# Kernel tuning notes

Measured on AMD Instinct MI355X. Metric: run time of the kernel, lower is better.

## Reference

```python
import jax, jax.numpy as jnp
import numpy as np

DIM = 1024
NUM_HEADS = 16
HEAD_DIM = DIM // NUM_HEADS


def setup_inputs() -> dict:
    key = jax.random.key(0)
    k1, k2, k3, k4, k5 = jax.random.split(key, 5)
    B, N, C = 8, 1024, DIM
    x = jax.random.normal(k1, (B, N, C), dtype=jnp.float32)
    s_in = 1.0 / np.sqrt(C)
    w_qkv = jax.random.normal(k2, (C, 3 * C), dtype=jnp.float32) * s_in
    b_qkv = jnp.zeros((3 * C,), dtype=jnp.float32)
    w_proj = jax.random.normal(k3, (C, C), dtype=jnp.float32) * s_in
    b_proj = jnp.zeros((C,), dtype=jnp.float32)
    return {"x": x, "w_qkv": w_qkv, "b_qkv": b_qkv, "w_proj": w_proj, "b_proj": b_proj}


def reference(x, w_qkv, b_qkv, w_proj, b_proj):
    B, N, C = x.shape
    H, D = NUM_HEADS, C // NUM_HEADS
    scale = jnp.float32(1.0) / jnp.sqrt(jnp.float32(D))
    qkv = x @ w_qkv + b_qkv                      # [B, N, 3C]
    qkv = qkv.reshape(B, N, 3, H, D)
    qkv = jnp.transpose(qkv, (2, 0, 3, 1, 4))     # [3, B, H, N, D]
    q, k, v = qkv[0], qkv[1], qkv[2]
    attn = jnp.einsum('bhnd,bhmd->bhnm', q, k) * scale  # [B, H, N, N]
    attn = jax.nn.softmax(attn, axis=-1)
    out = jnp.einsum('bhnm,bhmd->bhnd', attn, v)  # [B, H, N, D]
    out = jnp.transpose(out, (0, 2, 1, 3)).reshape(B, N, C)
    return out @ w_proj + b_proj
```

## Files before the change

### kernel.cpp

```cpp
#include <hip/hip_runtime.h>
#include <stdint.h>
#include <stddef.h>


#define DEVI __device__ __forceinline__

typedef float f32x4 __attribute__((ext_vector_type(4)));
typedef float f32x16 __attribute__((ext_vector_type(16)));
typedef __bf16 bf16x8 __attribute__((ext_vector_type(8)));
typedef unsigned short u16x8 __attribute__((ext_vector_type(8)));
typedef unsigned short u16x4 __attribute__((ext_vector_type(4)));
typedef unsigned int u32;
typedef unsigned int u32x4 __attribute__((ext_vector_type(4)));

static constexpr int M1 = 8192;

DEVI unsigned short f2bf(float f) {
  uint32_t u = __builtin_bit_cast(uint32_t, f);
  u += 0x7FFFu + ((u >> 16) & 1u);
  return (unsigned short)(u >> 16);
}

DEVI float fexp2(float x) {
  float r;
  asm("v_exp_f32 %0, %1" : "=v"(r) : "v"(x));
  return r;
}

DEVI u32 cvtpk(float lo, float hi) {
  u32 r;
  asm("v_cvt_pk_bf16_f32 %0, %1, %2" : "=v"(r) : "v"(lo), "v"(hi));
  return r;
}

DEVI void plswap(u32& a, u32& b) {
  asm("v_permlane32_swap_b32 %0, %1" : "+v"(a), "+v"(b));
}

DEVI void gll16(const unsigned short* g, unsigned short* lds) {
  __builtin_amdgcn_global_load_lds(
      (const __attribute__((address_space(1))) void*)g,
      (__attribute__((address_space(3))) void*)lds, 16, 0, 0);
}

DEVI bf16x8 lds_frag(const unsigned short* p) {
  return __builtin_bit_cast(bf16x8, *(const u16x8*)p);
}

__global__ void k_cvt(const float* __restrict__ in, unsigned short* __restrict__ out, int n4) {
  int i = blockIdx.x * blockDim.x + threadIdx.x;
  if (i < n4) {
    float4 v = reinterpret_cast<const float4*>(in)[i];
    u16x4 o = { f2bf(v.x), f2bf(v.y), f2bf(v.z), f2bf(v.w) };
    reinterpret_cast<u16x4*>(out)[i] = o;
  }
}

__global__ void k_tr_cvt(const float* __restrict__ in, unsigned short* __restrict__ out,
                         int R, int Cc) {
  __shared__ float tile[32][33];
  int c0 = blockIdx.x * 32, r0 = blockIdx.y * 32;
  int tx = threadIdx.x, ty = threadIdx.y;
#pragma unroll
  for (int j = 0; j < 32; j += 8)
    tile[ty + j][tx] = in[(size_t)(r0 + ty + j) * Cc + c0 + tx];
  __syncthreads();
#pragma unroll
  for (int j = 0; j < 32; j += 8)
    out[(size_t)(c0 + ty + j) * R + r0 + tx] = f2bf(tile[tx][ty + j]);
}

template <int EPI, int NCOLS>
__global__ __launch_bounds__(256, 2)
void k_gemm(const unsigned short* __restrict__ A,
            const unsigned short* __restrict__ Bt,
            const float* __restrict__ bias,
            unsigned short* __restrict__ Qp,
            unsigned short* __restrict__ Kp,
            unsigned short* __restrict__ Vtp,
            float* __restrict__ Out) {
  constexpr int K = 1024, NK = K / 32;
  __shared__ unsigned short As[2][128 * 32];
  __shared__ unsigned short Bs[2][128 * 32];

  const int tid = threadIdx.x;
  const int w = tid >> 6, l = tid & 63;
  const int ln = l & 15, kg = l >> 4;
  const int wr = w >> 1, wc = w & 1;

  const int rt = blockIdx.x % (M1 / 128);
  const int ct = blockIdx.x / (M1 / 128);
  const int row0 = rt * 128, col0 = ct * 128;

  f32x4 acc[4][4] = {};

  const unsigned short* Ag = A + (size_t)row0 * K;
  const unsigned short* Bg = Bt + (size_t)col0 * K;

  auto stage = [&](int buf, int kt) {
    const unsigned short* ga = Ag + kt * 32;
    const unsigned short* gb = Bg + kt * 32;
#pragma unroll
    for (int j = 0; j < 2; j++) {
      int c = j * 256 + w * 64 + l;
      int r = c >> 2, s = c & 3;
      int ss = s ^ ((r >> 1) & 3);
      gll16(ga + (size_t)r * K + ss * 8, &As[buf][(j * 256 + w * 64) * 8]);
      gll16(gb + (size_t)r * K + ss * 8, &Bs[buf][(j * 256 + w * 64) * 8]);
    }
  };

  stage(0, 0);
  __syncthreads();

  int buf = 0;
  for (int kt = 0; kt < NK; kt++) {
    if (kt + 1 < NK) stage(buf ^ 1, kt + 1);

    bf16x8 af[4], bfr[4];
#pragma unroll
    for (int m = 0; m < 4; m++) {
      int r = wr * 64 + m * 16 + ln;
      int sl = kg ^ ((r >> 1) & 3);
      af[m] = lds_frag(&As[buf][r * 32 + sl * 8]);
    }
#pragma unroll
    for (int n = 0; n < 4; n++) {
      int r = wc * 64 + n * 16 + ln;
      int sl = kg ^ ((r >> 1) & 3);
      bfr[n] = lds_frag(&Bs[buf][r * 32 + sl * 8]);
    }
    __builtin_amdgcn_s_setprio(1);
#pragma unroll
    for (int m = 0; m < 4; m++)
#pragma unroll
      for (int n = 0; n < 4; n++)
        acc[m][n] = __builtin_amdgcn_mfma_f32_16x16x32_bf16(af[m], bfr[n], acc[m][n], 0, 0, 0);
    __builtin_amdgcn_s_setprio(0);

    __syncthreads();
    buf ^= 1;
  }

  constexpr float QS = 0.18033688011112042f;
  float bv[4];
#pragma unroll
  for (int n = 0; n < 4; n++) bv[n] = bias[col0 + wc * 64 + n * 16 + ln];

  if constexpr (EPI == 1) {
    const int three = col0 >> 10;
    const int h = ((col0 & 1023) >> 6) + wc;
    if (three < 2) {
      unsigned short* tgt = (three == 0) ? Qp : Kp;
      const float sc = (three == 0) ? QS : 1.f;
#pragma unroll
      for (int m = 0; m < 4; m++)
#pragma unroll
        for (int r = 0; r < 4; r++) {
          int row = row0 + wr * 64 + m * 16 + kg * 4 + r;
          int bb = row >> 10, nn = row & 1023;
          size_t base = ((size_t)(bb * 16 + h) * 1024 + nn) * 64;
#pragma unroll
          for (int n = 0; n < 4; n++)
            tgt[base + n * 16 + ln] = f2bf((acc[m][n][r] + bv[n]) * sc);
        }
    } else {
#pragma unroll
      for (int m = 0; m < 4; m++)
#pragma unroll
        for (int r = 0; r < 4; r++) {
          int row = row0 + wr * 64 + m * 16 + kg * 4 + r;
          int bb = row >> 10, nn = row & 1023;
          size_t dbase = (size_t)(bb * 16 + h) * 64;
#pragma unroll
          for (int n = 0; n < 4; n++)
            Vtp[(dbase + n * 16 + ln) * 1024 + nn] = f2bf(acc[m][n][r] + bv[n]);
        }
    }
  } else {
#pragma unroll
    for (int m = 0; m < 4; m++)
#pragma unroll
      for (int r = 0; r < 4; r++) {
        int row = row0 + wr * 64 + m * 16 + kg * 4 + r;
#pragma unroll
        for (int n = 0; n < 4; n++)
          Out[(size_t)row * 1024 + col0 + wc * 64 + n * 16 + ln] = acc[m][n][r] + bv[n];
      }
  }
}

__global__ __launch_bounds__(256, 4)
void k_attn(const unsigned short* __restrict__ Qg, const unsigned short* __restrict__ Kg,
            const unsigned short* __restrict__ Vtg, unsigned short* __restrict__ AO) {
  __shared__ unsigned short Ks[2][64 * 64];
  __shared__ unsigned short Vs[2][64 * 64];

  const int tid = threadIdx.x;
  const int w = tid >> 6, l = tid & 63;
  const int lq = l & 31, b = l >> 5;

  const int bh = blockIdx.x;
  const int qt = blockIdx.y;
  const int qbase = qt * 128 + w * 32;

  bf16x8 qf[4];
#pragma unroll
  for (int kk = 0; kk < 4; kk++) {
    size_t off = ((size_t)bh * 1024 + qbase + lq) * 64 + kk * 16 + b * 8;
    qf[kk] = __builtin_bit_cast(bf16x8, *(const u16x8*)(Qg + off));
  }

  f32x16 acc[2] = {};
  float mrun = -1e30f, lrun = 0.f;

  const unsigned short* Kbh = Kg + (size_t)bh * 1024 * 64;
  const unsigned short* Vbh = Vtg + (size_t)bh * 64 * 1024;

  auto stage = [&](int buf, int t) {
#pragma unroll
    for (int j = 0; j < 2; j++) {
      int c = j * 256 + w * 64 + l;
      int r = c >> 3, s = c & 7;
      int ss = s ^ (r & 7);
      gll16(Kbh + (size_t)(t * 64 + r) * 64 + ss * 8, &Ks[buf][(j * 256 + w * 64) * 8]);
      gll16(Vbh + (size_t)r * 1024 + t * 64 + ss * 8, &Vs[buf][(j * 256 + w * 64) * 8]);
    }
  };

  stage(0, 0);
  __syncthreads();

  int buf = 0;
  for (int t = 0; t < 16; t++) {
    if (t + 1 < 16) stage(buf ^ 1, t + 1);

    f32x16 s[2];
    __builtin_amdgcn_s_setprio(1);
#pragma unroll
    for (int kb = 0; kb < 2; kb++) {
      f32x16 z = {};
#pragma unroll
      for (int kk = 0; kk < 4; kk++) {
        int row = kb * 32 + lq;
        int ss = (kk * 2 + b) ^ (row & 7);
        bf16x8 kf = lds_frag(&Ks[buf][row * 64 + ss * 8]);
        z = __builtin_amdgcn_mfma_f32_32x32x16_bf16(kf, qf[kk], z, 0, 0, 0);
      }
      s[kb] = z;
    }
    __builtin_amdgcn_s_setprio(0);

    float tm = s[0][0];
#pragma unroll
    for (int kb = 0; kb < 2; kb++)
#pragma unroll
      for (int r = 0; r < 16; r++) tm = fmaxf(tm, s[kb][r]);
    tm = fmaxf(tm, __shfl_xor(tm, 32));

    if (!__all(tm <= mrun + 8.f)) {
      float mnew = fmaxf(mrun, tm);
      float al = fexp2(mrun - mnew);
      mrun = mnew;
      lrun *= al;
#pragma unroll
      for (int r = 0; r < 16; r++) {
        float aq = __shfl(al, (r & 3) + 8 * (r >> 2) + 4 * b);
        acc[0][r] *= aq;
        acc[1][r] *= aq;
      }
    }

    float rs = 0.f;
#pragma unroll
    for (int kb = 0; kb < 2; kb++)
#pragma unroll
      for (int r = 0; r < 16; r++) {
        float pv = fexp2(s[kb][r] - mrun);
        s[kb][r] = pv;
        rs += pv;
      }
    rs += __shfl_xor(rs, 32);
    lrun += rs;

    bf16x8 pa[4];
#pragma unroll
    for (int kb = 0; kb < 2; kb++) {
      u32 pk[4][2];
#pragma unroll
      for (int t4 = 0; t4 < 4; t4++) {
        pk[t4][0] = cvtpk(s[kb][t4 * 4 + 0], s[kb][t4 * 4 + 1]);
        pk[t4][1] = cvtpk(s[kb][t4 * 4 + 2], s[kb][t4 * 4 + 3]);
      }
#pragma unroll
      for (int sh = 0; sh < 2; sh++) {
        u32 a0 = pk[2 * sh][0], b0 = pk[2 * sh + 1][0];
        plswap(a0, b0);
        u32 a1 = pk[2 * sh][1], b1 = pk[2 * sh + 1][1];
        plswap(a1, b1);
        u32x4 fr = { a0, a1, b0, b1 };
        pa[kb * 2 + sh] = __builtin_bit_cast(bf16x8, fr);
      }
    }

    __builtin_amdgcn_s_setprio(1);
#pragma unroll
    for (int n = 0; n < 2; n++) {
#pragma unroll
      for (int st = 0; st < 4; st++) {
        int row = n * 32 + lq;
        int ss = (st * 2 + b) ^ (row & 7);
        bf16x8 vb = lds_frag(&Vs[buf][row * 64 + ss * 8]);
        acc[n] = __builtin_amdgcn_mfma_f32_32x32x16_bf16(pa[st], vb, acc[n], 0, 0, 0);
      }
    }
    __builtin_amdgcn_s_setprio(0);

    __syncthreads();
    buf ^= 1;
  }

  const int bb = bh >> 4, h = bh & 15;
  float linv = 1.f / lrun;
#pragma unroll
  for (int r = 0; r < 16; r++) {
    float lq_r = __shfl(linv, (r & 3) + 8 * (r >> 2) + 4 * b);
    int row = qbase + (r & 3) + 8 * (r >> 2) + 4 * b;
    size_t base = ((size_t)(bb * 1024 + row)) * 1024 + h * 64;
#pragma unroll
    for (int n = 0; n < 2; n++)
      AO[base + n * 32 + lq] = f2bf(acc[n][r] * lq_r);
  }
}

extern "C" void kernel_launch(void* const* d_in, const int* in_sizes, int n_in,
                              void* d_out, int out_size, void* d_ws, size_t ws_size,
                              hipStream_t stream) {
  const float* x      = (const float*)d_in[0];
  const float* w_qkv  = (const float*)d_in[1];
  const float* b_qkv  = (const float*)d_in[2];
  const float* w_proj = (const float*)d_in[3];
  const float* b_proj = (const float*)d_in[4];
  float* out = (float*)d_out;

  constexpr size_t SZ_XB  = (size_t)8192 * 1024 * 2;
  constexpr size_t SZ_WQ  = (size_t)3072 * 1024 * 2;
  constexpr size_t SZ_WP  = (size_t)1024 * 1024 * 2;
  constexpr size_t SZ_QKV = (size_t)8 * 16 * 1024 * 64 * 2;
  char* ws = (char*)d_ws;
  unsigned short* xb     = (unsigned short*)(ws);
  unsigned short* wqkvT  = (unsigned short*)(ws + SZ_XB);
  unsigned short* wprojT = (unsigned short*)(ws + SZ_XB + SZ_WQ);
  unsigned short* Qb     = (unsigned short*)(ws + SZ_XB + SZ_WQ + SZ_WP);
  unsigned short* Kb     = (unsigned short*)(ws + SZ_XB + SZ_WQ + SZ_WP + SZ_QKV);
  unsigned short* Vtb    = (unsigned short*)(ws + SZ_XB + SZ_WQ + SZ_WP + 2 * SZ_QKV);
  unsigned short* AOb    = (unsigned short*)(ws + SZ_XB + SZ_WQ + SZ_WP + 3 * SZ_QKV);
  size_t needed = SZ_XB + SZ_WQ + SZ_WP + 4 * SZ_QKV;
  if (ws_size < needed) return;

  k_cvt<<<8192, 256, 0, stream>>>(x, xb, 8192 * 1024 / 4);
  dim3 tb(32, 8);
  k_tr_cvt<<<dim3(96, 32), tb, 0, stream>>>(w_qkv, wqkvT, 1024, 3072);
  k_tr_cvt<<<dim3(32, 32), tb, 0, stream>>>(w_proj, wprojT, 1024, 1024);
  k_gemm<1, 3072><<<64 * 24, 256, 0, stream>>>(xb, wqkvT, b_qkv, Qb, Kb, Vtb, nullptr);
  k_attn<<<dim3(128, 8), 256, 0, stream>>>(Qb, Kb, Vtb, AOb);
  k_gemm<2, 1024><<<64 * 8, 256, 0, stream>>>(AOb, wprojT, b_proj, nullptr, nullptr, nullptr, out);
}
```

Measured before the change: 240.1 us.

## Fuse fp32-to-bf16 conversion of x into QKV GEMM loads; merge weight prep kernels

Removes the separate x conversion kernel: the QKV GEMM now loads fp32 x directly from global memory into registers, converts to bf16 and writes the swizzled tile to LDS after the MFMA work, overlapping the load with compute. The two weight transpose kernels are merged into one launch. This avoids writing and rereading a 16MB bf16 copy of x and saves launches, but the A operand is read from global memory 24 times as fp32 (double bytes), uses more registers, and loses the async global_load_lds path for A.

Result: slower. 250.4 us (+4.3%).

```diff
diff --git a/kernel.cpp b/kernel.cpp
--- a/kernel.cpp
+++ b/kernel.cpp
@@ -47,38 +47,168 @@
   return __builtin_bit_cast(bf16x8, *(const u16x8*)p);
 }
 
-__global__ void k_cvt(const float* __restrict__ in, unsigned short* __restrict__ out, int n4) {
-  int i = blockIdx.x * blockDim.x + threadIdx.x;
-  if (i < n4) {
-    float4 v = reinterpret_cast<const float4*>(in)[i];
-    u16x4 o = { f2bf(v.x), f2bf(v.y), f2bf(v.z), f2bf(v.w) };
-    reinterpret_cast<u16x4*>(out)[i] = o;
-  }
-}
-
-__global__ void k_tr_cvt(const float* __restrict__ in, unsigned short* __restrict__ out,
-                         int R, int Cc) {
+__global__ void k_prep(const float* __restrict__ wqkv, const float* __restrict__ wproj,
+                       unsigned short* __restrict__ wqkvT, unsigned short* __restrict__ wprojT) {
   __shared__ float tile[32][33];
-  int c0 = blockIdx.x * 32, r0 = blockIdx.y * 32;
-  int tx = threadIdx.x, ty = threadIdx.y;
+  const int bx = blockIdx.x;
+  const float* in = (bx < 96) ? wqkv : wproj;
+  unsigned short* out = (bx < 96) ? wqkvT : wprojT;
+  const int Cc = (bx < 96) ? 3072 : 1024;
+  const int c0 = ((bx < 96) ? bx : bx - 96) * 32, r0 = blockIdx.y * 32;
+  const int tx = threadIdx.x, ty = threadIdx.y;
 #pragma unroll
   for (int j = 0; j < 32; j += 8)
     tile[ty + j][tx] = in[(size_t)(r0 + ty + j) * Cc + c0 + tx];
   __syncthreads();
 #pragma unroll
   for (int j = 0; j < 32; j += 8)
-    out[(size_t)(c0 + ty + j) * R + r0 + tx] = f2bf(tile[tx][ty + j]);
-}
-
-template <int EPI, int NCOLS>
+    out[(size_t)(c0 + ty + j) * 1024 + r0 + tx] = f2bf(tile[tx][ty + j]);
+}
+
 __global__ __launch_bounds__(256, 2)
-void k_gemm(const unsigned short* __restrict__ A,
-            const unsigned short* __restrict__ Bt,
-            const float* __restrict__ bias,
-            unsigned short* __restrict__ Qp,
-            unsigned short* __restrict__ Kp,
-            unsigned short* __restrict__ Vtp,
-            float* __restrict__ Out) {
+void k_gemm1(const float* __restrict__ X,
+             const unsigned short* __restrict__ Bt,
+             const float* __restrict__ bias,
+             unsigned short* __restrict__ Qp,
+             unsigned short* __restrict__ Kp,
+             unsigned short* __restrict__ Vtp) {
+  constexpr int K = 1024, NK = K / 32;
+  __shared__ unsigned short As[2][128 * 32];
+  __shared__ unsigned short Bs[2][128 * 32];
+
+  const int tid = threadIdx.x;
+  const int w = tid >> 6, l = tid & 63;
+  const int ln = l & 15, kg = l >> 4;
+  const int wr = w >> 1, wc = w & 1;
+
+  const int rt = blockIdx.x % (M1 / 128);
+  const int ct = blockIdx.x / (M1 / 128);
+  const int row0 = rt * 128, col0 = ct * 128;
+
+  f32x4 acc[4][4] = {};
+
+  const float* Ag = X + (size_t)row0 * K;
+  const unsigned short* Bg = Bt + (size_t)col0 * K;
+
+  int cr[2], cs[2], cd[2];
+#pragma unroll
+  for (int j = 0; j < 2; j++) {
+    int c = j * 256 + w * 64 + l;
+    cr[j] = c >> 2; cs[j] = c & 3;
+    cd[j] = cr[j] * 4 + (cs[j] ^ ((cr[j] >> 1) & 3));
+  }
+
+  auto loadA = [&](int kt, float4* a0, float4* a1) {
+#pragma unroll
+    for (int j = 0; j < 2; j++) {
+      const float* src = Ag + (size_t)cr[j] * K + kt * 32 + cs[j] * 8;
+      a0[j] = *(const float4*)src;
+      a1[j] = *(const float4*)(src + 4);
+    }
+  };
+  auto writeA = [&](int buf, const float4* a0, const float4* a1) {
+#pragma unroll
+    for (int j = 0; j < 2; j++) {
+      u16x8 p = { f2bf(a0[j].x), f2bf(a0[j].y), f2bf(a0[j].z), f2bf(a0[j].w),
+                  f2bf(a1[j].x), f2bf(a1[j].y), f2bf(a1[j].z), f2bf(a1[j].w) };
+      *(u16x8*)&As[buf][cd[j] * 8] = p;
+    }
+  };
+  auto stageB = [&](int buf, int kt) {
+    const unsigned short* gb = Bg + kt * 32;
+#pragma unroll
+    for (int j = 0; j < 2; j++) {
+      int c = j * 256 + w * 64 + l;
+      int r = c >> 2, s = c & 3;
+      int ss = s ^ ((r >> 1) & 3);
+      gll16(gb + (size_t)r * K + ss * 8, &Bs[buf][(j * 256 + w * 64) * 8]);
+    }
+  };
+
+  {
+    float4 a0[2], a1[2];
+    loadA(0, a0, a1);
+    writeA(0, a0, a1);
+    stageB(0, 0);
+  }
+  __syncthreads();
+
+  int buf = 0;
+  for (int kt = 0; kt < NK; kt++) {
+    float4 a0[2], a1[2];
+    if (kt + 1 < NK) {
+      loadA(kt + 1, a0, a1);
+      stageB(buf ^ 1, kt + 1);
+    }
+    __builtin_amdgcn_sched_barrier(0);
+
+    bf16x8 af[4], bfr[4];
+#pragma unroll
+    for (int m = 0; m < 4; m++) {
+      int r = wr * 64 + m * 16 + ln;
+      int sl = kg ^ ((r >> 1) & 3);
+      af[m] = lds_frag(&As[buf][r * 32 + sl * 8]);
+    }
+#pragma unroll
+    for (int n = 0; n < 4; n++) {
+      int r = wc * 64 + n * 16 + ln;
+      int sl = kg ^ ((r >> 1) & 3);
+      bfr[n] = lds_frag(&Bs[buf][r * 32 + sl * 8]);
+    }
+    __builtin_amdgcn_s_setprio(1);
+#pragma unroll
+    for (int m = 0; m < 4; m++)
+#pragma unroll
+      for (int n = 0; n < 4; n++)
+        acc[m][n] = __builtin_amdgcn_mfma_f32_16x16x32_bf16(af[m], bfr[n], acc[m][n], 0, 0, 0);
+    __builtin_amdgcn_s_setprio(0);
+
+    if (kt + 1 < NK) writeA(buf ^ 1, a0, a1);
+    __syncthreads();
+    buf ^= 1;
+  }
+
+  constexpr float QS = 0.18033688011112042f;
+  float bv[4];
+#pragma unroll
+  for (int n = 0; n < 4; n++) bv[n] = bias[col0 + wc * 64 + n * 16 + ln];
+
+  const int three = col0 >> 10;
+  const int h = ((col0 & 1023) >> 6) + wc;
+  if (three < 2) {
+    unsigned short* tgt = (three == 0) ? Qp : Kp;
+    const float sc = (three == 0) ? QS : 1.f;
+#pragma unroll
+    for (int m = 0; m < 4; m++)
+#pragma unroll
+      for (int r = 0; r < 4; r++) {
+        int row = row0 + wr * 64 + m * 16 + kg * 4 + r;
+        int bb = row >> 10, nn = row & 1023;
+        size_t base = ((size_t)(bb * 16 + h) * 1024 + nn) * 64;
+#pragma unroll
+        for (int n = 0; n < 4; n++)
+          tgt[base + n * 16 + ln] = f2bf((acc[m][n][r] + bv[n]) * sc);
+      }
+  } else {
+#pragma unroll
+    for (int m = 0; m < 4; m++)
+#pragma unroll
+      for (int r = 0; r < 4; r++) {
+        int row = row0 + wr * 64 + m * 16 + kg * 4 + r;
+        int bb = row >> 10, nn = row & 1023;
+        size_t dbase = (size_t)(bb * 16 + h) * 64;
+#pragma unroll
+        for (int n = 0; n < 4; n++)
+          Vtp[(dbase + n * 16 + ln) * 1024 + nn] = f2bf(acc[m][n][r] + bv[n]);
+      }
+  }
+}
+
+__global__ __launch_bounds__(256, 2)
+void k_gemm2(const unsigned short* __restrict__ A,
+             const unsigned short* __restrict__ Bt,
+             const float* __restrict__ bias,
+             float* __restrict__ Out) {
   constexpr int K = 1024, NK = K / 32;
   __shared__ unsigned short As[2][128 * 32];
   __shared__ unsigned short Bs[2][128 * 32];
@@ -142,52 +272,18 @@
     buf ^= 1;
   }
 
-  constexpr float QS = 0.18033688011112042f;
   float bv[4];
 #pragma unroll
   for (int n = 0; n < 4; n++) bv[n] = bias[col0 + wc * 64 + n * 16 + ln];
-
-  if constexpr (EPI == 1) {
-    const int three = col0 >> 10;
-    const int h = ((col0 & 1023) >> 6) + wc;
-    if (three < 2) {
-      unsigned short* tgt = (three == 0) ? Qp : Kp;
-      const float sc = (three == 0) ? QS : 1.f;
-#pragma unroll
-      for (int m = 0; m < 4; m++)
-#pragma unroll
-        for (int r = 0; r < 4; r++) {
-          int row = row0 + wr * 64 + m * 16 + kg * 4 + r;
-          int bb = row >> 10, nn = row & 1023;
-          size_t base = ((size_t)(bb * 16 + h) * 1024 + nn) * 64;
-#pragma unroll
-          for (int n = 0; n < 4; n++)
-            tgt[base + n * 16 + ln] = f2bf((acc[m][n][r] + bv[n]) * sc);
-        }
-    } else {
-#pragma unroll
-      for (int m = 0; m < 4; m++)
-#pragma unroll
-        for (int r = 0; r < 4; r++) {
-          int row = row0 + wr * 64 + m * 16 + kg * 4 + r;
-          int bb = row >> 10, nn = row & 1023;
-          size_t dbase = (size_t)(bb * 16 + h) * 64;
-#pragma unroll
-          for (int n = 0; n < 4; n++)
-            Vtp[(dbase + n * 16 + ln) * 1024 + nn] = f2bf(acc[m][n][r] + bv[n]);
-        }
-    }
-  } else {
-#pragma unroll
-    for (int m = 0; m < 4; m++)
-#pragma unroll
-      for (int r = 0; r < 4; r++) {
-        int row = row0 + wr * 64 + m * 16 + kg * 4 + r;
-#pragma unroll
-        for (int n = 0; n < 4; n++)
-          Out[(size_t)row * 1024 + col0 + wc * 64 + n * 16 + ln] = acc[m][n][r] + bv[n];
-      }
-  }
+#pragma unroll
+  for (int m = 0; m < 4; m++)
+#pragma unroll
+    for (int r = 0; r < 4; r++) {
+      int row = row0 + wr * 64 + m * 16 + kg * 4 + r;
+#pragma unroll
+      for (int n = 0; n < 4; n++)
+        Out[(size_t)row * 1024 + col0 + wc * 64 + n * 16 + ln] = acc[m][n][r] + bv[n];
+    }
 }
 
 __global__ __launch_bounds__(256, 4)
@@ -343,26 +439,21 @@
   const float* b_proj = (const float*)d_in[4];
   float* out = (float*)d_out;
 
-  constexpr size_t SZ_XB  = (size_t)8192 * 1024 * 2;
   constexpr size_t SZ_WQ  = (size_t)3072 * 1024 * 2;
   constexpr size_t SZ_WP  = (size_t)1024 * 1024 * 2;
   constexpr size_t SZ_QKV = (size_t)8 * 16 * 1024 * 64 * 2;
   char* ws = (char*)d_ws;
-  unsigned short* xb     = (unsigned short*)(ws);
-  unsigned short* wqkvT  = (unsigned short*)(ws + SZ_XB);
-  unsigned short* wprojT = (unsigned short*)(ws + SZ_XB + SZ_WQ);
-  unsigned short* Qb     = (unsigned short*)(ws + SZ_XB + SZ_WQ + SZ_WP);
-  unsigned short* Kb     = (unsigned short*)(ws + SZ_XB + SZ_WQ + SZ_WP + SZ_QKV);
-  unsigned short* Vtb    = (unsigned short*)(ws + SZ_XB + SZ_WQ + SZ_WP + 2 * SZ_QKV);
-  unsigned short* AOb    = (unsigned short*)(ws + SZ_XB + SZ_WQ + SZ_WP + 3 * SZ_QKV);
-  size_t needed = SZ_XB + SZ_WQ + SZ_WP + 4 * SZ_QKV;
+  unsigned short* wqkvT  = (unsigned short*)(ws);
+  unsigned short* wprojT = (unsigned short*)(ws + SZ_WQ);
+  unsigned short* Qb     = (unsigned short*)(ws + SZ_WQ + SZ_WP);
+  unsigned short* Kb     = (unsigned short*)(ws + SZ_WQ + SZ_WP + SZ_QKV);
+  unsigned short* Vtb    = (unsigned short*)(ws + SZ_WQ + SZ_WP + 2 * SZ_QKV);
+  unsigned short* AOb    = (unsigned short*)(ws + SZ_WQ + SZ_WP + 3 * SZ_QKV);
+  size_t needed = SZ_WQ + SZ_WP + 4 * SZ_QKV;
   if (ws_size < needed) return;
 
-  k_cvt<<<8192, 256, 0, stream>>>(x, xb, 8192 * 1024 / 4);
-  dim3 tb(32, 8);
-  k_tr_cvt<<<dim3(96, 32), tb, 0, stream>>>(w_qkv, wqkvT, 1024, 3072);
-  k_tr_cvt<<<dim3(32, 32), tb, 0, stream>>>(w_proj, wprojT, 1024, 1024);
-  k_gemm<1, 3072><<<64 * 24, 256, 0, stream>>>(xb, wqkvT, b_qkv, Qb, Kb, Vtb, nullptr);
+  k_prep<<<dim3(128, 32), dim3(32, 8), 0, stream>>>(w_qkv, w_proj, wqkvT, wprojT);
+  k_gemm1<<<64 * 24, 256, 0, stream>>>(x, wqkvT, b_qkv, Qb, Kb, Vtb);
   k_attn<<<dim3(128, 8), 256, 0, stream>>>(Qb, Kb, Vtb, AOb);
-  k_gemm<2, 1024><<<64 * 8, 256, 0, stream>>>(AOb, wprojT, b_proj, nullptr, nullptr, nullptr, out);
-}
+  k_gemm2<<<64 * 8, 256, 0, stream>>>(AOb, wprojT, b_proj, out);
+}
```
